# Kernel tuning notes

Measured on AMD Instinct MI355X. Metric: run time of the kernel, lower is better.

The kernel has to match this reference:

```python
import jax, jax.numpy as jnp
import numpy as np

HIDDEN = 512
HEADS = 8
HEAD_DIM = HIDDEN // HEADS


def setup_inputs() -> dict:
    key = jax.random.key(0)
    ks = jax.random.split(key, 9)
    B, S = 4, 2048
    scale = 1.0 / np.sqrt(HIDDEN)
    x = jax.random.normal(ks[0], (B, S, HIDDEN), dtype=jnp.float32)
    Wq = jax.random.normal(ks[1], (HIDDEN, HIDDEN), dtype=jnp.float32) * scale
    Wk = jax.random.normal(ks[2], (HIDDEN, HIDDEN), dtype=jnp.float32) * scale
    Wv = jax.random.normal(ks[3], (HIDDEN, HIDDEN), dtype=jnp.float32) * scale
    Wo = jax.random.normal(ks[4], (HIDDEN, HIDDEN), dtype=jnp.float32) * scale
    bq = jax.random.normal(ks[5], (HIDDEN,), dtype=jnp.float32) * 0.01
    bk = jax.random.normal(ks[6], (HIDDEN,), dtype=jnp.float32) * 0.01
    bv = jax.random.normal(ks[7], (HIDDEN,), dtype=jnp.float32) * 0.01
    bo = jax.random.normal(ks[8], (HIDDEN,), dtype=jnp.float32) * 0.01
    return {"x": x, "Wq": Wq, "bq": bq, "Wk": Wk, "bk": bk,
            "Wv": Wv, "bv": bv, "Wo": Wo, "bo": bo}


def reference(x, Wq, bq, Wk, bk, Wv, bv, Wo, bo):
    B, S, _ = x.shape
    # project and split heads: [B, H, S, D]
    def split_heads(t):
        return t.reshape(B, S, HEADS, HEAD_DIM).transpose(0, 2, 1, 3)
    Q = split_heads(x @ Wq.T + bq)
    K = split_heads(x @ Wk.T + bk)
    V = split_heads(x @ Wv.T + bv)
    scores = jnp.einsum("bhsd,bhtd->bhst", Q, K) / jnp.sqrt(
        jnp.array(HEAD_DIM, dtype=x.dtype))
    attn = jax.nn.softmax(scores, axis=-1)  # dropout is identity in eval
    ctx = jnp.einsum("bhst,bhtd->bhsd", attn, V)
    ctx = ctx.transpose(0, 2, 1, 3).reshape(B, S, HIDDEN)
    return ctx @ Wo.T + bo
```

## Files before the change

kernel.cpp:

```cpp
#include <hip/hip_runtime.h>
#include <stdint.h>

#define HID 512
#define NH 8
#define HD 64
#define BB 4
#define SS 2048

typedef unsigned short u16;
typedef __attribute__((ext_vector_type(8))) short short8;
typedef __attribute__((ext_vector_type(4))) float f32x4;
typedef __attribute__((ext_vector_type(4))) _Float16 f16x4;
typedef __attribute__((ext_vector_type(8))) _Float16 f16x8;
typedef __attribute__((ext_vector_type(2))) unsigned int uint2v;
typedef __attribute__((ext_vector_type(4))) unsigned int uint4v;

#define MFMA16(a, b, c) __builtin_amdgcn_mfma_f32_16x16x32_bf16((a), (b), (c), 0, 0, 0)
#define MFMAH32(a, b, c) __builtin_amdgcn_mfma_f32_16x16x32_f16((a), (b), (c), 0, 0, 0)

#define WAIT_VM4() __builtin_amdgcn_s_waitcnt(0xF74)
#define WAIT_VM3() __builtin_amdgcn_s_waitcnt(0xF73)
#define WAIT_VM0() __builtin_amdgcn_s_waitcnt(0xF70)
#define PIPE_BARRIER() do { asm volatile("" ::: "memory"); \
  __builtin_amdgcn_s_barrier(); asm volatile("" ::: "memory"); } while (0)

__device__ __forceinline__ u16 f2bf(float f) {
  union { float f; uint32_t u; } v; v.f = f;
  return (u16)((v.u + 0x7fffu + ((v.u >> 16) & 1u)) >> 16);
}

__device__ __forceinline__ u16 f2h(float f) {
  _Float16 h = (_Float16)f;
  return __builtin_bit_cast(u16, h);
}

__device__ __forceinline__ void gl_lds16(const u16* g, u16* l) {
  __builtin_amdgcn_global_load_lds(
      (const __attribute__((address_space(1))) unsigned int*)g,
      (__attribute__((address_space(3))) unsigned int*)l, 16, 0, 0);
}

__global__ void prep(const float* __restrict__ x,
                     const float* __restrict__ w0, const float* __restrict__ w1,
                     const float* __restrict__ w2, const float* __restrict__ w3,
                     u16* __restrict__ xb,
                     u16* __restrict__ o0, u16* __restrict__ o1,
                     u16* __restrict__ o2, u16* __restrict__ o3) {
  const int bid = blockIdx.x;
  const float* in;
  u16* out;
  int base;
  if (bid < 2048) {
    in = x; out = xb; base = bid * 2048;
  } else {
    const int z = (bid - 2048) >> 7;
    base = ((bid - 2048) & 127) * 2048;
    in = (z == 0) ? w0 : (z == 1) ? w1 : (z == 2) ? w2 : w3;
    out = (z == 0) ? o0 : (z == 1) ? o1 : (z == 2) ? o2 : o3;
  }
  const int i = base + threadIdx.x * 8;
  float4 v0 = *(const float4*)(in + i);
  float4 v1 = *(const float4*)(in + i + 4);
  ushort4 a, b;
  a.x = f2bf(v0.x); a.y = f2bf(v0.y); a.z = f2bf(v0.z); a.w = f2bf(v0.w);
  b.x = f2bf(v1.x); b.y = f2bf(v1.y); b.z = f2bf(v1.z); b.w = f2bf(v1.w);
  *(ushort4*)(out + i) = a;
  *(ushort4*)(out + i + 4) = b;
}

__global__ __launch_bounds__(256, 3)
void qkv_gemm(const u16* __restrict__ xb,
              const u16* __restrict__ wq, const u16* __restrict__ wk, const u16* __restrict__ wv,
              const float* __restrict__ bq, const float* __restrict__ bk, const float* __restrict__ bv,
              u16* __restrict__ Q, u16* __restrict__ K, u16* __restrict__ Vt) {
  __shared__ u16 sA[3][4096];
  __shared__ u16 sB[3][4096];
  const int tid = threadIdx.x;
  const int lane = tid & 63;
  const int wave = tid >> 6;
  const int l15 = lane & 15;
  const int quad = lane >> 4;
  const int wm = wave >> 1, wn = wave & 1;

  const int L = blockIdx.x;
  const int xcd = L & 7;
  const int slot = L >> 3;
  const int bm = xcd * 8 + (slot & 7);
  const int r2 = slot >> 3;
  const int bn = r2 & 3;
  const int z = r2 >> 2;

  const float* bias = (z == 0) ? bq : (z == 1) ? bk : bv;
  const float scale = (z == 0) ? 0.18033688011112042f : 1.0f;

  const u16* Arows = (z == 2) ? wv : xb;
  const u16* Brows = (z == 2) ? xb : ((z == 0) ? wq : wk);
  const int am0 = (z == 2) ? (bn * 128) : (bm * 128);
  const int bn0 = (z == 2) ? (bm * 128) : (bn * 128);

  const int srow = tid >> 2;
  const int sg = (tid & 3) ^ ((srow >> 1) & 3);
  const u16* gA = Arows + (am0 + srow) * 512 + sg * 8;
  const u16* gB = Brows + (bn0 + srow) * 512 + sg * 8;

  const int fsw = (quad ^ ((l15 >> 1) & 3)) * 8;
  int aoff[4], boff[4];
#pragma unroll
  for (int t = 0; t < 4; ++t) {
    aoff[t] = (wm * 64 + t * 16 + l15) * 32 + fsw;
    boff[t] = (wn * 64 + t * 16 + l15) * 32 + fsw;
  }

  f32x4 acc[4][4] = {};

#pragma unroll
  for (int t = 0; t < 2; ++t) {
    const int k0 = t * 32;
    gl_lds16(gA + k0, &sA[t][wave * 512]);
    gl_lds16(gA + k0 + 64 * 512, &sA[t][2048 + wave * 512]);
    gl_lds16(gB + k0, &sB[t][wave * 512]);
    gl_lds16(gB + k0 + 64 * 512, &sB[t][2048 + wave * 512]);
  }

  for (int kk = 0; kk < 16; ++kk) {
    WAIT_VM4();
    PIPE_BARRIER();
    {
      const int tp = (kk + 2 < 16) ? kk + 2 : 15;
      const int ns = (kk + 2) % 3;
      const int k0 = tp * 32;
      gl_lds16(gA + k0, &sA[ns][wave * 512]);
      gl_lds16(gA + k0 + 64 * 512, &sA[ns][2048 + wave * 512]);
      gl_lds16(gB + k0, &sB[ns][wave * 512]);
      gl_lds16(gB + k0 + 64 * 512, &sB[ns][2048 + wave * 512]);
    }
    const int cur = kk % 3;
    short8 af[4], bf[4];
#pragma unroll
    for (int t = 0; t < 4; ++t) af[t] = *(const short8*)&sA[cur][aoff[t]];
#pragma unroll
    for (int t = 0; t < 4; ++t) bf[t] = *(const short8*)&sB[cur][boff[t]];
#pragma unroll
    for (int mi = 0; mi < 4; ++mi)
#pragma unroll
      for (int ni = 0; ni < 4; ++ni)
        acc[mi][ni] = MFMA16(af[mi], bf[ni], acc[mi][ni]);
  }

  if (z != 2) {
    u16* dst = (z == 0) ? Q : K;
#pragma unroll
    for (int mi = 0; mi < 4; ++mi) {
#pragma unroll
      for (int ni = 0; ni < 4; ++ni) {
        const int col = bn0 + wn * 64 + ni * 16 + l15;
        const float bs = bias[col];
#pragma unroll
        for (int i = 0; i < 4; ++i) {
          const int row = am0 + wm * 64 + mi * 16 + quad * 4 + i;
          const float v = (acc[mi][ni][i] + bs) * scale;
          const int b = row >> 11, s = row & 2047;
          const int h = col >> 6, d = col & 63;
          dst[(((size_t)(b * 8 + h) * 2048 + s) << 6) + d] = f2bf(v);
        }
      }
    }
  } else {
#pragma unroll
    for (int mi = 0; mi < 4; ++mi) {
#pragma unroll
      for (int i = 0; i < 4; ++i) {
        const int o = am0 + wm * 64 + mi * 16 + quad * 4 + i;
        const float bs = bias[o];
        const int h = o >> 6, d = o & 63;
#pragma unroll
        for (int ni = 0; ni < 4; ++ni) {
          const int r = bn0 + wn * 64 + ni * 16 + l15;
          const int b = r >> 11, s = r & 2047;
          Vt[(((size_t)(b * 8 + h) * 64 + d) << 11) + s] = f2h(acc[mi][ni][i] + bs);
        }
      }
    }
  }
}

__global__ __launch_bounds__(512, 4)
void attn(const u16* __restrict__ Q, const u16* __restrict__ K,
          const u16* __restrict__ Vt, u16* __restrict__ ctx) {
  __shared__ __align__(16) u16 smem[4 * 8192];
  const int tid = threadIdx.x;
  const int lane = tid & 63;
  const int wave = tid >> 6;
  const int l15 = lane & 15;
  const int quad = lane >> 4;
  const int pair = wave >> 1;
  const int par = wave & 1;

  const int L = blockIdx.x;
  const int xcd = L & 7;
  const int slotb = L >> 3;
  const int bh = xcd * 4 + (slotb & 3);
  const int qt = slotb >> 2;

  const u16* Qb = Q + (size_t)bh * SS * HD;
  const u16* Kb = K + (size_t)bh * SS * HD;
  const u16* Vb = Vt + (size_t)bh * HD * SS;

  const int rowbase = qt * 128 + pair * 32;
  short8 qf[2][2];
#pragma unroll
  for (int rf = 0; rf < 2; ++rf)
#pragma unroll
    for (int kc = 0; kc < 2; ++kc)
      qf[rf][kc] = *(const short8*)(Qb + (rowbase + rf * 16 + l15) * 64 + kc * 32 + quad * 8);
  asm volatile("" ::: "memory");

  f32x4 oacc[2][4] = {};
  float plsum[2] = {0.f, 0.f};

  const int trow = tid >> 3;
  const int rK = (trow & 3) | (((trow >> 3) & 1) << 2);
  const int gswK = (tid & 7) ^ rK;
  const int gswV = (tid & 7) ^ (trow & 7);
  const int kOff = trow * 64 + gswK * 8;
  const int vOff = trow * 2048 + gswV * 8;
  u16* ldsK = smem + tid * 8;
  u16* ldsV = smem + 4096 + tid * 8;

  const int l7 = l15 & 7;
  const int tKbase = par * 32 + ((l15 >> 2) * 8) + (l15 & 3);
  int kfo[2][2];
#pragma unroll
  for (int s = 0; s < 2; ++s)
#pragma unroll
    for (int kc = 0; kc < 2; ++kc)
      kfo[s][kc] = (tKbase + 4 * s) * 64 + (((kc * 4 + quad) ^ l7) * 8);
  const int vfoV = l15 * 64 + (((par * 4 + quad) ^ l7) * 8);

#pragma unroll
  for (int t = 0; t < 3; ++t) {
    gl_lds16(Kb + t * 4096 + kOff, ldsK + t * 8192);
    gl_lds16(Vb + t * 64 + vOff, ldsV + t * 8192);
  }

  for (int tt = 0; tt < 32; ++tt) {
    WAIT_VM4();
    PIPE_BARRIER();
    {
      const int tp = (tt + 3 < 32) ? tt + 3 : 31;
      const int ns = (tt + 3) & 3;
      gl_lds16(Kb + tp * 4096 + kOff, ldsK + ns * 8192);
      gl_lds16(Vb + tp * 64 + vOff, ldsV + ns * 8192);
    }
    const int cb = (tt & 3) * 8192;

    short8 ks[2][2];
#pragma unroll
    for (int s = 0; s < 2; ++s)
#pragma unroll
      for (int kc = 0; kc < 2; ++kc)
        ks[s][kc] = *(const short8*)&smem[cb + kfo[s][kc]];
    f32x4 sacc[2][2] = {};
    __builtin_amdgcn_s_setprio(1);
#pragma unroll
    for (int s = 0; s < 2; ++s)
#pragma unroll
      for (int rf = 0; rf < 2; ++rf) {
        sacc[s][rf] = MFMA16(ks[s][0], qf[rf][0], sacc[s][rf]);
        sacc[s][rf] = MFMA16(ks[s][1], qf[rf][1], sacc[s][rf]);
      }
    __builtin_amdgcn_s_setprio(0);
    short8 vraw[4];
#pragma unroll
    for (int nd = 0; nd < 4; ++nd)
      vraw[nd] = *(const short8*)&smem[cb + 4096 + nd * 1024 + vfoV];
#pragma unroll
    for (int rf = 0; rf < 2; ++rf) {
      const float p0 = __builtin_amdgcn_exp2f(sacc[0][rf][0]);
      const float p1 = __builtin_amdgcn_exp2f(sacc[0][rf][1]);
      const float p2 = __builtin_amdgcn_exp2f(sacc[0][rf][2]);
      const float p3 = __builtin_amdgcn_exp2f(sacc[0][rf][3]);
      const float p4 = __builtin_amdgcn_exp2f(sacc[1][rf][0]);
      const float p5 = __builtin_amdgcn_exp2f(sacc[1][rf][1]);
      const float p6 = __builtin_amdgcn_exp2f(sacc[1][rf][2]);
      const float p7 = __builtin_amdgcn_exp2f(sacc[1][rf][3]);
      plsum[rf] += ((p0 + p1) + (p2 + p3)) + ((p4 + p5) + (p6 + p7));
      uint4v pw;
      pw.x = __builtin_bit_cast(unsigned int, __builtin_amdgcn_cvt_pkrtz(p0, p1));
      pw.y = __builtin_bit_cast(unsigned int, __builtin_amdgcn_cvt_pkrtz(p2, p3));
      pw.z = __builtin_bit_cast(unsigned int, __builtin_amdgcn_cvt_pkrtz(p4, p5));
      pw.w = __builtin_bit_cast(unsigned int, __builtin_amdgcn_cvt_pkrtz(p6, p7));
      const f16x8 pf = __builtin_bit_cast(f16x8, pw);
      __builtin_amdgcn_s_setprio(1);
#pragma unroll
      for (int nd = 0; nd < 4; ++nd)
        oacc[rf][nd] = MFMAH32(pf, __builtin_bit_cast(f16x8, vraw[nd]), oacc[rf][nd]);
      __builtin_amdgcn_s_setprio(0);
    }
  }

  WAIT_VM0();
  __syncthreads();

#pragma unroll
  for (int rf = 0; rf < 2; ++rf) {
    plsum[rf] += __shfl_xor(plsum[rf], 16);
    plsum[rf] += __shfl_xor(plsum[rf], 32);
  }

  float* cbuf = (float*)smem;
  float* lbuf = cbuf + 128 * 68;
  if (par) {
#pragma unroll
    for (int rf = 0; rf < 2; ++rf) {
#pragma unroll
      for (int nd = 0; nd < 4; ++nd)
#pragma unroll
        for (int i = 0; i < 4; ++i)
          cbuf[(pair * 32 + rf * 16 + quad * 4 + i) * 68 + nd * 16 + l15] = oacc[rf][nd][i];
      if (quad == 0) lbuf[pair * 32 + rf * 16 + l15] = plsum[rf];
    }
  }
  __syncthreads();
  if (!par) {
    const int b = bh >> 3, h = bh & 7;
#pragma unroll
    for (int rf = 0; rf < 2; ++rf) {
      const float tot = plsum[rf] + lbuf[pair * 32 + rf * 16 + l15];
      float inv[4];
#pragma unroll
      for (int i = 0; i < 4; ++i)
        inv[i] = __builtin_amdgcn_rcpf(__shfl(tot, quad * 4 + i));
#pragma unroll
      for (int nd = 0; nd < 4; ++nd)
#pragma unroll
        for (int i = 0; i < 4; ++i) {
          const float v = (oacc[rf][nd][i] +
                           cbuf[(pair * 32 + rf * 16 + quad * 4 + i) * 68 + nd * 16 + l15]) * inv[i];
          const int s = rowbase + rf * 16 + quad * 4 + i;
          const int d = nd * 16 + l15;
          ctx[((size_t)(b * 2048 + s) << 9) + h * 64 + d] = f2bf(v);
        }
    }
  }
}

__global__ __launch_bounds__(256, 2)
void out_gemm(const u16* __restrict__ A, const u16* __restrict__ W,
              const float* __restrict__ bias, float* __restrict__ out) {
  __shared__ u16 sA[3][4096];
  __shared__ u16 sB[3][2048];
  const int tid = threadIdx.x;
  const int lane = tid & 63;
  const int wave = tid >> 6;
  const int l15 = lane & 15;
  const int quad = lane >> 4;

  const int L = blockIdx.x;
  const int xcd = L & 7;
  const int slot = L >> 3;
  const int bm = xcd * 8 + (slot & 7);
  const int bn = slot >> 3;

  const int srow = tid >> 2;
  const int sg = (tid & 3) ^ ((srow >> 1) & 3);
  const u16* gA = A + (bm * 128 + srow) * 512 + sg * 8;
  const u16* gB = W + (bn * 64 + srow) * 512 + sg * 8;

  const int fsw = (quad ^ ((l15 >> 1) & 3)) * 8;
  int aoff[2], boff[4];
#pragma unroll
  for (int t = 0; t < 2; ++t) aoff[t] = (wave * 32 + t * 16 + l15) * 32 + fsw;
#pragma unroll
  for (int t = 0; t < 4; ++t) boff[t] = (t * 16 + l15) * 32 + fsw;

  f32x4 acc[2][4] = {};

#pragma unroll
  for (int t = 0; t < 2; ++t) {
    const int k0 = t * 32;
    gl_lds16(gA + k0, &sA[t][wave * 512]);
    gl_lds16(gA + k0 + 64 * 512, &sA[t][2048 + wave * 512]);
    gl_lds16(gB + k0, &sB[t][wave * 512]);
  }

  for (int kk = 0; kk < 16; ++kk) {
    WAIT_VM3();
    PIPE_BARRIER();
    {
      const int tp = (kk + 2 < 16) ? kk + 2 : 15;
      const int ns = (kk + 2) % 3;
      const int k0 = tp * 32;
      gl_lds16(gA + k0, &sA[ns][wave * 512]);
      gl_lds16(gA + k0 + 64 * 512, &sA[ns][2048 + wave * 512]);
      gl_lds16(gB + k0, &sB[ns][wave * 512]);
    }
    const int cur = kk % 3;
    short8 af[2], bf[4];
#pragma unroll
    for (int t = 0; t < 2; ++t) af[t] = *(const short8*)&sA[cur][aoff[t]];
#pragma unroll
    for (int t = 0; t < 4; ++t) bf[t] = *(const short8*)&sB[cur][boff[t]];
#pragma unroll
    for (int mi = 0; mi < 2; ++mi)
#pragma unroll
      for (int ni = 0; ni < 4; ++ni)
        acc[mi][ni] = MFMA16(af[mi], bf[ni], acc[mi][ni]);
  }

#pragma unroll
  for (int mi = 0; mi < 2; ++mi) {
#pragma unroll
    for (int ni = 0; ni < 4; ++ni) {
      const int col = bn * 64 + ni * 16 + l15;
      const float bs = bias[col];
#pragma unroll
      for (int i = 0; i < 4; ++i) {
        const int row = bm * 128 + wave * 32 + mi * 16 + quad * 4 + i;
        out[(size_t)row * 512 + col] = acc[mi][ni][i] + bs;
      }
    }
  }
}

extern "C" void kernel_launch(void* const* d_in, const int* in_sizes, int n_in,
                              void* d_out, int out_size, void* d_ws, size_t ws_size,
                              hipStream_t stream) {
  const float* x = (const float*)d_in[0];
  const float* Wq = (const float*)d_in[1];
  const float* bq = (const float*)d_in[2];
  const float* Wk = (const float*)d_in[3];
  const float* bk = (const float*)d_in[4];
  const float* Wv = (const float*)d_in[5];
  const float* bv = (const float*)d_in[6];
  const float* Wo = (const float*)d_in[7];
  const float* bo = (const float*)d_in[8];
  float* out = (float*)d_out;

  char* ws = (char*)d_ws;
  u16* xb  = (u16*)(ws);
  u16* wqb = (u16*)(ws + (8u << 20));
  u16* wkb = (u16*)(ws + (8u << 20) + (512u << 10));
  u16* wvb = (u16*)(ws + (9u << 20));
  u16* wob = (u16*)(ws + (9u << 20) + (512u << 10));
  u16* Qb  = (u16*)(ws + (10u << 20));
  u16* Kb  = (u16*)(ws + (18u << 20));
  u16* Vtb = (u16*)(ws + (26u << 20));
  u16* ctx = (u16*)(ws + (34u << 20));

  prep<<<2560, 256, 0, stream>>>(x, Wq, Wk, Wv, Wo, xb, wqb, wkb, wvb, wob);
  qkv_gemm<<<768, 256, 0, stream>>>(xb, wqb, wkb, wvb, bq, bk, bv, Qb, Kb, Vtb);
  attn<<<512, 512, 0, stream>>>(Qb, Kb, Vtb, ctx);
  out_gemm<<<512, 256, 0, stream>>>(ctx, wob, bo, out);
}
```

Before: 156.1 us.

## Software-pipeline attention loop: compute next QK scores while processing previous PV

Restructures the attention main loop into a prologue, a steady state and an epilogue, so each iteration computes exp and the PV MFMAs for the previous tile while issuing the QK MFMAs for the current tile. This is meant to hide the exp/convert latency behind the score MFMAs and to raise matrix-unit utilization. The waitcnt also now waits on LDS counters explicitly. Extra live registers for the carried scores and V fragments may raise register pressure and hurt occupancy.

```diff
diff --git a/kernel.cpp b/kernel.cpp
--- a/kernel.cpp
+++ b/kernel.cpp
@@ -21,6 +21,7 @@
 #define WAIT_VM4() __builtin_amdgcn_s_waitcnt(0xF74)
 #define WAIT_VM3() __builtin_amdgcn_s_waitcnt(0xF73)
 #define WAIT_VM0() __builtin_amdgcn_s_waitcnt(0xF70)
+#define WAIT_VM4_LG0() __builtin_amdgcn_s_waitcnt(0x074)
 #define PIPE_BARRIER() do { asm volatile("" ::: "memory"); \
   __builtin_amdgcn_s_barrier(); asm volatile("" ::: "memory"); } while (0)
 
@@ -243,14 +244,47 @@
     gl_lds16(Vb + t * 64 + vOff, ldsV + t * 8192);
   }
 
-  for (int tt = 0; tt < 32; ++tt) {
-    WAIT_VM4();
+  f32x4 psacc[2][2];
+  short8 pvraw[4];
+
+  {
+    WAIT_VM4_LG0();
+    PIPE_BARRIER();
+    gl_lds16(Kb + 3 * 4096 + kOff, ldsK + 3 * 8192);
+    gl_lds16(Vb + 3 * 64 + vOff, ldsV + 3 * 8192);
+    short8 ks[2][2];
+#pragma unroll
+    for (int s = 0; s < 2; ++s)
+#pragma unroll
+      for (int kc = 0; kc < 2; ++kc)
+        ks[s][kc] = *(const short8*)&smem[kfo[s][kc]];
+    f32x4 ns[2][2] = {};
+    __builtin_amdgcn_s_setprio(1);
+#pragma unroll
+    for (int s = 0; s < 2; ++s)
+#pragma unroll
+      for (int rf = 0; rf < 2; ++rf) {
+        ns[s][rf] = MFMA16(ks[s][0], qf[rf][0], ns[s][rf]);
+        ns[s][rf] = MFMA16(ks[s][1], qf[rf][1], ns[s][rf]);
+      }
+    __builtin_amdgcn_s_setprio(0);
+#pragma unroll
+    for (int s = 0; s < 2; ++s)
+#pragma unroll
+      for (int rf = 0; rf < 2; ++rf) psacc[s][rf] = ns[s][rf];
+#pragma unroll
+    for (int nd = 0; nd < 4; ++nd)
+      pvraw[nd] = *(const short8*)&smem[4096 + nd * 1024 + vfoV];
+  }
+
+  for (int tt = 1; tt < 32; ++tt) {
+    WAIT_VM4_LG0();
     PIPE_BARRIER();
     {
       const int tp = (tt + 3 < 32) ? tt + 3 : 31;
-      const int ns = (tt + 3) & 3;
-      gl_lds16(Kb + tp * 4096 + kOff, ldsK + ns * 8192);
-      gl_lds16(Vb + tp * 64 + vOff, ldsV + ns * 8192);
+      const int ns2 = (tt + 3) & 3;
+      gl_lds16(Kb + tp * 4096 + kOff, ldsK + ns2 * 8192);
+      gl_lds16(Vb + tp * 64 + vOff, ldsV + ns2 * 8192);
     }
     const int cb = (tt & 3) * 8192;
 
@@ -260,30 +294,17 @@
 #pragma unroll
       for (int kc = 0; kc < 2; ++kc)
         ks[s][kc] = *(const short8*)&smem[cb + kfo[s][kc]];
-    f32x4 sacc[2][2] = {};
-    __builtin_amdgcn_s_setprio(1);
-#pragma unroll
-    for (int s = 0; s < 2; ++s)
-#pragma unroll
-      for (int rf = 0; rf < 2; ++rf) {
-        sacc[s][rf] = MFMA16(ks[s][0], qf[rf][0], sacc[s][rf]);
-        sacc[s][rf] = MFMA16(ks[s][1], qf[rf][1], sacc[s][rf]);
-      }
-    __builtin_amdgcn_s_setprio(0);
-    short8 vraw[4];
-#pragma unroll
-    for (int nd = 0; nd < 4; ++nd)
-      vraw[nd] = *(const short8*)&smem[cb + 4096 + nd * 1024 + vfoV];
+
 #pragma unroll
     for (int rf = 0; rf < 2; ++rf) {
-      const float p0 = __builtin_amdgcn_exp2f(sacc[0][rf][0]);
-      const float p1 = __builtin_amdgcn_exp2f(sacc[0][rf][1]);
-      const float p2 = __builtin_amdgcn_exp2f(sacc[0][rf][2]);
-      const float p3 = __builtin_amdgcn_exp2f(sacc[0][rf][3]);
-      const float p4 = __builtin_amdgcn_exp2f(sacc[1][rf][0]);
-      const float p5 = __builtin_amdgcn_exp2f(sacc[1][rf][1]);
-      const float p6 = __builtin_amdgcn_exp2f(sacc[1][rf][2]);
-      const float p7 = __builtin_amdgcn_exp2f(sacc[1][rf][3]);
+      const float p0 = __builtin_amdgcn_exp2f(psacc[0][rf][0]);
+      const float p1 = __builtin_amdgcn_exp2f(psacc[0][rf][1]);
+      const float p2 = __builtin_amdgcn_exp2f(psacc[0][rf][2]);
+      const float p3 = __builtin_amdgcn_exp2f(psacc[0][rf][3]);
+      const float p4 = __builtin_amdgcn_exp2f(psacc[1][rf][0]);
+      const float p5 = __builtin_amdgcn_exp2f(psacc[1][rf][1]);
+      const float p6 = __builtin_amdgcn_exp2f(psacc[1][rf][2]);
+      const float p7 = __builtin_amdgcn_exp2f(psacc[1][rf][3]);
       plsum[rf] += ((p0 + p1) + (p2 + p3)) + ((p4 + p5) + (p6 + p7));
       uint4v pw;
       pw.x = __builtin_bit_cast(unsigned int, __builtin_amdgcn_cvt_pkrtz(p0, p1));
@@ -291,15 +312,56 @@
       pw.z = __builtin_bit_cast(unsigned int, __builtin_amdgcn_cvt_pkrtz(p4, p5));
       pw.w = __builtin_bit_cast(unsigned int, __builtin_amdgcn_cvt_pkrtz(p6, p7));
       const f16x8 pf = __builtin_bit_cast(f16x8, pw);
-      __builtin_amdgcn_s_setprio(1);
 #pragma unroll
       for (int nd = 0; nd < 4; ++nd)
-        oacc[rf][nd] = MFMAH32(pf, __builtin_bit_cast(f16x8, vraw[nd]), oacc[rf][nd]);
-      __builtin_amdgcn_s_setprio(0);
-    }
-  }
-
-  WAIT_VM0();
+        oacc[rf][nd] = MFMAH32(pf, __builtin_bit_cast(f16x8, pvraw[nd]), oacc[rf][nd]);
+    }
+
+    f32x4 nsacc[2][2] = {};
+    __builtin_amdgcn_s_setprio(1);
+#pragma unroll
+    for (int s = 0; s < 2; ++s)
+#pragma unroll
+      for (int rf = 0; rf < 2; ++rf) {
+        nsacc[s][rf] = MFMA16(ks[s][0], qf[rf][0], nsacc[s][rf]);
+        nsacc[s][rf] = MFMA16(ks[s][1], qf[rf][1], nsacc[s][rf]);
+      }
+    __builtin_amdgcn_s_setprio(0);
+
+#pragma unroll
+    for (int s = 0; s < 2; ++s)
+#pragma unroll
+      for (int rf = 0; rf < 2; ++rf) psacc[s][rf] = nsacc[s][rf];
+#pragma unroll
+    for (int nd = 0; nd < 4; ++nd)
+      pvraw[nd] = *(const short8*)&smem[cb + 4096 + nd * 1024 + vfoV];
+  }
+
+  {
+    WAIT_VM0();
+#pragma unroll
+    for (int rf = 0; rf < 2; ++rf) {
+      const float p0 = __builtin_amdgcn_exp2f(psacc[0][rf][0]);
+      const float p1 = __builtin_amdgcn_exp2f(psacc[0][rf][1]);
+      const float p2 = __builtin_amdgcn_exp2f(psacc[0][rf][2]);
+      const float p3 = __builtin_amdgcn_exp2f(psacc[0][rf][3]);
+      const float p4 = __builtin_amdgcn_exp2f(psacc[1][rf][0]);
+      const float p5 = __builtin_amdgcn_exp2f(psacc[1][rf][1]);
+      const float p6 = __builtin_amdgcn_exp2f(psacc[1][rf][2]);
+      const float p7 = __builtin_amdgcn_exp2f(psacc[1][rf][3]);
+      plsum[rf] += ((p0 + p1) + (p2 + p3)) + ((p4 + p5) + (p6 + p7));
+      uint4v pw;
+      pw.x = __builtin_bit_cast(unsigned int, __builtin_amdgcn_cvt_pkrtz(p0, p1));
+      pw.y = __builtin_bit_cast(unsigned int, __builtin_amdgcn_cvt_pkrtz(p2, p3));
+      pw.z = __builtin_bit_cast(unsigned int, __builtin_amdgcn_cvt_pkrtz(p4, p5));
+      pw.w = __builtin_bit_cast(unsigned int, __builtin_amdgcn_cvt_pkrtz(p6, p7));
+      const f16x8 pf = __builtin_bit_cast(f16x8, pw);
+#pragma unroll
+      for (int nd = 0; nd < 4; ++nd)
+        oacc[rf][nd] = MFMAH32(pf, __builtin_bit_cast(f16x8, pvraw[nd]), oacc[rf][nd]);
+    }
+  }
+
   __syncthreads();
 
 #pragma unroll
```

Result: no change. 158.8 us (+1.7%).
